# Kernel optimization log

Measured on AMD Instinct MI355X. Metric: run time of the kernel, lower is better.

The kernel has to match this reference:

```python
import jax, jax.numpy as jnp
import numpy as np

NUM_FIELDS = 16
EMBED = 32
W1 = 7
W2 = 5
VOCAB = 100000
BATCH = 4096
K1 = NUM_FIELDS // 2  # first k-max pool size (num_inputs/2)
K2 = 3                # second k-max pool size
DN = ('NHWC', 'HWIO', 'NHWC')


def kmax_pool_last(x, k):
    # k-max pooling along the last axis (tf.nn.top_k values)
    return jax.lax.top_k(x, k)[0]


def setup_inputs() -> dict:
    key = jax.random.key(0)
    ks = jax.random.split(key, 6)
    return {
        'idx': jax.random.randint(ks[0], (BATCH, NUM_FIELDS), 0, VOCAB),
        'w0': jax.random.normal(ks[1], (NUM_FIELDS, VOCAB, EMBED), jnp.float32) * 0.02,
        'b0': jnp.zeros((NUM_FIELDS, EMBED), jnp.float32),
        'f1': jax.random.normal(ks[2], (EMBED, W1, 1, 2), jnp.float32) * 0.1,
        'f2': jax.random.normal(ks[3], (EMBED, W2, 2, 2), jnp.float32) * 0.1,
        'w1': jax.random.normal(ks[4], (2 * 3 * EMBED, 1), jnp.float32) * 0.02,
        'b1': jnp.zeros((1,), jnp.float32),
    }


def reference(idx, w0, b0, f1, f2, w1, b1):
    # sparse one-hot matmul == embedding row gather: [B, F, E]
    emb = w0[jnp.arange(NUM_FIELDS)[None, :], idx] + b0[None, :, :]
    l = jnp.tanh(emb)  # layer_acts[0] = tanh; dropout identity at test
    # reshape [-1, F, E, 1] then transpose [0,2,1,3] -> [B, E, F, 1]
    l = jnp.transpose(l[..., None], (0, 2, 1, 3))
    # conv1: kernel [E, W1, 1, 2], SAME -> [B, E, F, 2]
    l = jax.lax.conv_general_dilated(l, f1, (1, 1), 'SAME', dimension_numbers=DN)
    # k-max pool over field axis (last axis after transpose) -> [B, E, K1, 2]
    l = jnp.transpose(kmax_pool_last(jnp.transpose(l, (0, 1, 3, 2)), K1), (0, 1, 3, 2))
    # conv2: kernel [E, W2, 2, 2], SAME -> [B, E, K1, 2]
    l = jax.lax.conv_general_dilated(l, f2, (1, 1), 'SAME', dimension_numbers=DN)
    # second k-max pool -> [B, E, 3, 2]
    l = jnp.transpose(kmax_pool_last(jnp.transpose(l, (0, 1, 3, 2)), K2), (0, 1, 3, 2))
    l = jnp.tanh(l.reshape(l.shape[0], EMBED * 3 * 2))  # layer_acts[1] = tanh
    logits = (l @ w1 + b1).reshape(-1)  # layer_acts[2] = none
    return jax.nn.sigmoid(logits)  # y_prob
```

## Files before the change

### kernel.cpp

```cpp
#include <hip/hip_runtime.h>
#include <math.h>

#define NF 16
#define VOCAB 100000
#define S1 28
#define NP1 31
#define PB 868
#define S2 20
#define LDSW 1736

typedef _Float16 h2 __attribute__((ext_vector_type(2)));

#if __has_builtin(__builtin_amdgcn_fdot2)
#define FDOT2(a, b, c) __builtin_amdgcn_fdot2((a), (b), (c), false)
#else
#define FDOT2(a, b, c) ((float)(a)[0] * (float)(b)[0] + ((float)(a)[1] * (float)(b)[1] + (c)))
#endif

__device__ __forceinline__ float tanhf_fast(float x) {
    float e = __expf(2.f * x);
    return 1.f - 2.f * __builtin_amdgcn_rcpf(e + 1.f);
}

__device__ __forceinline__ h2 u2h(unsigned int u) {
    union { unsigned int u; h2 h; } c; c.u = u; return c.h;
}

__global__ void pack_filters(const float* __restrict__ f1,
                             const float* __restrict__ f2,
                             unsigned int* __restrict__ ws) {
    int t = threadIdx.x;
    if (t < 224) {
        int j = t / 14, r = t % 14, kw = r >> 1, o = r & 1;
        h2 h;
        h[0] = (_Float16)f1[((2 * j) * 7 + kw) * 2 + o];
        h[1] = (_Float16)f1[((2 * j + 1) * 7 + kw) * 2 + o];
        union { h2 h; unsigned int u; } c; c.h = h;
        ws[t] = c.u;
    }
    for (int n = t; n < 320; n += 256) {
        int kh = n / 10, r = n % 10, kw = r >> 1, o = r & 1;
        h2 h;
        h[0] = (_Float16)f2[(kh * 5 + kw) * 4 + o];
        h[1] = (_Float16)f2[(kh * 5 + kw) * 4 + 2 + o];
        union { h2 h; unsigned int u; } c; c.h = h;
        ws[256 + n] = c.u;
    }
}

__global__ __launch_bounds__(64, 4) void ccpm_fwd(
    const int* __restrict__ idx,
    const float* __restrict__ w0,
    const float* __restrict__ b0,
    const float* __restrict__ w1,
    const float* __restrict__ b1,
    const unsigned int* __restrict__ FP,
    float* __restrict__ out)
{
    const int b = blockIdx.x;
    const int l = threadIdx.x;

    __shared__ __align__(16) unsigned int lds[LDSW];

    const float4 z4 = make_float4(0.f, 0.f, 0.f, 0.f);

    #pragma unroll
    for (int i = 0; i < 7; ++i) {
        int n = i * 64 + l;
        if (n < LDSW / 4) ((float4*)lds)[n] = z4;
    }
    __syncthreads();

    {
        int f  = l >> 2;
        int e0 = (l & 3) * 8;
        int row = idx[b * NF + f];
        const float4* src = (const float4*)(w0 + ((size_t)f * VOCAB + row) * 32 + e0);
        const float4* bb  = (const float4*)(b0 + f * 32 + e0);
        float4 v0 = src[0], v1 = src[1];
        float4 u0 = bb[0],  u1 = bb[1];
        float g[8];
        g[0]=v0.x+u0.x; g[1]=v0.y+u0.y; g[2]=v0.z+u0.z; g[3]=v0.w+u0.w;
        g[4]=v1.x+u1.x; g[5]=v1.y+u1.y; g[6]=v1.z+u1.z; g[7]=v1.w+u1.w;
        _Float16* H = (_Float16*)lds;
        const int C = f + 3;
        #pragma unroll
        for (int i = 0; i < 8; ++i) {
            int R = e0 + i + 15;
            _Float16 hv = (_Float16)tanhf_fast(g[i]);
            H[((R >> 1) * S1 + C) * 2 + (R & 1)] = hv;
            int prB = (R & 1) ? (R >> 1) : (R >> 1) - 1;
            H[(PB + prB * S1 + C) * 2 + ((R & 1) ^ 1)] = hv;
        }
    }
    __syncthreads();

    const int h  = l >> 1;
    const int wh = l & 1;

    float a0[8], a1[8];
    {
        #pragma unroll
        for (int w = 0; w < 8; ++w) { a0[w] = 0.f; a1[w] = 0.f; }
        const unsigned int* plane = lds + ((h & 1) ? PB : 0);
        const int pr0 = h >> 1;
        const int wb  = wh * 8;
        #pragma unroll 2
        for (int j = 0; j < 16; ++j) {
            const uint4* rp = (const uint4*)(plane + (pr0 + j) * S1 + wb);
            uint4 q0 = rp[0], q1 = rp[1], q2 = rp[2], q3 = rp[3];
            unsigned int win[16] = {q0.x,q0.y,q0.z,q0.w, q1.x,q1.y,q1.z,q1.w,
                                    q2.x,q2.y,q2.z,q2.w, q3.x,q3.y,q3.z,q3.w};
            const unsigned int* ft = FP + j * 14;
            #pragma unroll
            for (int kw = 0; kw < 7; ++kw) {
                h2 f0 = u2h(ft[kw * 2 + 0]);
                h2 f1h = u2h(ft[kw * 2 + 1]);
                #pragma unroll
                for (int w = 0; w < 8; ++w) {
                    h2 wv = u2h(win[w + kw]);
                    a0[w] = FDOT2(wv, f0, a0[w]);
                    a1[w] = FDOT2(wv, f1h, a1[w]);
                }
            }
        }
    }
    __syncthreads();

    #pragma unroll
    for (int i = 0; i < 5; ++i) {
        int n = i * 64 + l;
        if (n < (63 * S2) / 4) ((float4*)lds)[n] = z4;
    }
    __syncthreads();

    {
        float own[8], recv[8];
        #pragma unroll
        for (int i = 0; i < 8; ++i) {
            own[i]  = wh ? a1[i] : a0[i];
            recv[i] = __shfl_xor(wh ? a0[i] : a1[i], 1, 64);
        }
        float v[16];
        #pragma unroll
        for (int i = 0; i < 8; ++i) {
            v[i]     = wh ? recv[i] : own[i];
            v[8 + i] = wh ? own[i] : recv[i];
        }
        int r[16];
        #pragma unroll
        for (int i = 0; i < 16; ++i) r[i] = 0;
        #pragma unroll
        for (int i = 0; i < 16; ++i)
            #pragma unroll
            for (int j = i + 1; j < 16; ++j) {
                bool ge = v[i] >= v[j];
                r[j] += ge ? 1 : 0;
                r[i] += ge ? 0 : 1;
            }
        _Float16* H = (_Float16*)lds;
        #pragma unroll
        for (int i = 0; i < 16; ++i)
            if (r[i] < 8)
                H[((h + 15) * S2 + (r[i] + 2)) * 2 + wh] = (_Float16)v[i];
    }
    __syncthreads();

    float c0[4], c1[4];
    {
        #pragma unroll
        for (int w = 0; w < 4; ++w) { c0[w] = 0.f; c1[w] = 0.f; }
        const int wb2 = wh * 4;
        #pragma unroll 2
        for (int kh = 0; kh < 32; ++kh) {
            const uint4* rp = (const uint4*)(lds + (h + kh) * S2 + wb2);
            uint4 qa = rp[0], qb = rp[1];
            unsigned int q[8] = {qa.x,qa.y,qa.z,qa.w, qb.x,qb.y,qb.z,qb.w};
            const unsigned int* ft = FP + 256 + kh * 10;
            #pragma unroll
            for (int kw = 0; kw < 5; ++kw) {
                h2 f0 = u2h(ft[kw * 2 + 0]);
                h2 f1h = u2h(ft[kw * 2 + 1]);
                #pragma unroll
                for (int w = 0; w < 4; ++w) {
                    h2 wv = u2h(q[w + kw]);
                    c0[w] = FDOT2(wv, f0, c0[w]);
                    c1[w] = FDOT2(wv, f1h, c1[w]);
                }
            }
        }
    }

    {
        float own[4], recv[4];
        #pragma unroll
        for (int i = 0; i < 4; ++i) {
            own[i]  = wh ? c1[i] : c0[i];
            recv[i] = __shfl_xor(wh ? c0[i] : c1[i], 1, 64);
        }
        float v[8];
        #pragma unroll
        for (int i = 0; i < 4; ++i) {
            v[i]     = wh ? recv[i] : own[i];
            v[4 + i] = wh ? own[i] : recv[i];
        }
        int r[8];
        #pragma unroll
        for (int i = 0; i < 8; ++i) r[i] = 0;
        #pragma unroll
        for (int i = 0; i < 8; ++i)
            #pragma unroll
            for (int j = i + 1; j < 8; ++j) {
                bool ge = v[i] >= v[j];
                r[j] += ge ? 1 : 0;
                r[i] += ge ? 0 : 1;
            }
        float t0 = 0.f, t1 = 0.f, t2 = 0.f;
        #pragma unroll
        for (int i = 0; i < 8; ++i) {
            t0 = (r[i] == 0) ? v[i] : t0;
            t1 = (r[i] == 1) ? v[i] : t1;
            t2 = (r[i] == 2) ? v[i] : t2;
        }
        float s = tanhf_fast(t0) * w1[h * 6 + wh]
                + tanhf_fast(t1) * w1[h * 6 + 2 + wh]
                + tanhf_fast(t2) * w1[h * 6 + 4 + wh];
        #pragma unroll
        for (int off = 32; off; off >>= 1) s += __shfl_xor(s, off, 64);
        if (l == 0) {
            float logit = s + b1[0];
            out[b] = __builtin_amdgcn_rcpf(1.f + __expf(-logit));
        }
    }
}

extern "C" void kernel_launch(void* const* d_in, const int* in_sizes, int n_in,
                              void* d_out, int out_size, void* d_ws, size_t ws_size,
                              hipStream_t stream) {
    const int*   idx = (const int*)d_in[0];
    const float* w0  = (const float*)d_in[1];
    const float* b0  = (const float*)d_in[2];
    const float* f1  = (const float*)d_in[3];
    const float* f2  = (const float*)d_in[4];
    const float* w1  = (const float*)d_in[5];
    const float* b1  = (const float*)d_in[6];
    float* out = (float*)d_out;
    unsigned int* ws = (unsigned int*)d_ws;

    pack_filters<<<1, 256, 0, stream>>>(f1, f2, ws);
    ccpm_fwd<<<out_size, 64, 0, stream>>>(idx, w0, b0, w1, b1, ws, out);
}
```

Baseline: 279.1 us.

## Split conv output channels across two wavefronts per sample with 128-thread blocks

Doubles the block to 128 threads so each wavefront computes one output channel of both convolutions, halving the per-thread accumulators and FDOT2 work. Filter packing is relaid out per output channel, and the two k-max pools now exchange data through cross-half shuffles (xor 32) instead of neighbour-lane shuffles. The final logit is combined across the two wavefronts through LDS with an extra barrier. This raises parallelism and lowers register pressure per sample, at the cost of duplicated sorting work in both halves and more block-level synchronisation.

```diff
diff --git a/kernel.cpp b/kernel.cpp
--- a/kernel.cpp
+++ b/kernel.cpp
@@ -4,10 +4,10 @@
 #define NF 16
 #define VOCAB 100000
 #define S1 28
-#define NP1 31
 #define PB 868
 #define S2 20
-#define LDSW 1736
+#define PLW 1736
+#define REDS 1700
 
 typedef _Float16 h2 __attribute__((ext_vector_type(2)));
 
@@ -31,24 +31,24 @@
                              unsigned int* __restrict__ ws) {
     int t = threadIdx.x;
     if (t < 224) {
-        int j = t / 14, r = t % 14, kw = r >> 1, o = r & 1;
+        int o = t / 112, r = t % 112, j = r / 7, kw = r % 7;
         h2 h;
         h[0] = (_Float16)f1[((2 * j) * 7 + kw) * 2 + o];
         h[1] = (_Float16)f1[((2 * j + 1) * 7 + kw) * 2 + o];
         union { h2 h; unsigned int u; } c; c.h = h;
-        ws[t] = c.u;
+        ws[o * 128 + j * 8 + kw] = c.u;
     }
     for (int n = t; n < 320; n += 256) {
-        int kh = n / 10, r = n % 10, kw = r >> 1, o = r & 1;
+        int o = n / 160, r = n % 160, kh = r / 5, kw = r % 5;
         h2 h;
         h[0] = (_Float16)f2[(kh * 5 + kw) * 4 + o];
         h[1] = (_Float16)f2[(kh * 5 + kw) * 4 + 2 + o];
         union { h2 h; unsigned int u; } c; c.h = h;
-        ws[256 + n] = c.u;
-    }
-}
-
-__global__ __launch_bounds__(64, 4) void ccpm_fwd(
+        ws[256 + o * 256 + kh * 8 + kw] = c.u;
+    }
+}
+
+__global__ __launch_bounds__(128, 8) void ccpm_fwd(
     const int* __restrict__ idx,
     const float* __restrict__ w0,
     const float* __restrict__ b0,
@@ -58,34 +58,30 @@
     float* __restrict__ out)
 {
     const int b = blockIdx.x;
-    const int l = threadIdx.x;
-
-    __shared__ __align__(16) unsigned int lds[LDSW];
+    const int t = threadIdx.x;
+
+    __shared__ __align__(16) unsigned int lds[PLW];
 
     const float4 z4 = make_float4(0.f, 0.f, 0.f, 0.f);
 
     #pragma unroll
-    for (int i = 0; i < 7; ++i) {
-        int n = i * 64 + l;
-        if (n < LDSW / 4) ((float4*)lds)[n] = z4;
-    }
-    __syncthreads();
-
-    {
-        int f  = l >> 2;
-        int e0 = (l & 3) * 8;
+    for (int i = 0; i < 4; ++i) {
+        int n = i * 128 + t;
+        if (n < PLW / 4) ((float4*)lds)[n] = z4;
+    }
+    __syncthreads();
+
+    {
+        int f  = t >> 3;
+        int e0 = (t & 7) * 4;
         int row = idx[b * NF + f];
-        const float4* src = (const float4*)(w0 + ((size_t)f * VOCAB + row) * 32 + e0);
-        const float4* bb  = (const float4*)(b0 + f * 32 + e0);
-        float4 v0 = src[0], v1 = src[1];
-        float4 u0 = bb[0],  u1 = bb[1];
-        float g[8];
-        g[0]=v0.x+u0.x; g[1]=v0.y+u0.y; g[2]=v0.z+u0.z; g[3]=v0.w+u0.w;
-        g[4]=v1.x+u1.x; g[5]=v1.y+u1.y; g[6]=v1.z+u1.z; g[7]=v1.w+u1.w;
+        float4 v = *(const float4*)(w0 + ((size_t)f * VOCAB + row) * 32 + e0);
+        float4 u = *(const float4*)(b0 + f * 32 + e0);
+        float g[4] = {v.x + u.x, v.y + u.y, v.z + u.z, v.w + u.w};
         _Float16* H = (_Float16*)lds;
         const int C = f + 3;
         #pragma unroll
-        for (int i = 0; i < 8; ++i) {
+        for (int i = 0; i < 4; ++i) {
             int R = e0 + i + 15;
             _Float16 hv = (_Float16)tanhf_fast(g[i]);
             H[((R >> 1) * S1 + C) * 2 + (R & 1)] = hv;
@@ -95,142 +91,137 @@
     }
     __syncthreads();
 
-    const int h  = l >> 1;
-    const int wh = l & 1;
-
-    float a0[8], a1[8];
-    {
-        #pragma unroll
-        for (int w = 0; w < 8; ++w) { a0[w] = 0.f; a1[w] = 0.f; }
+    const int h    = t & 31;
+    const int half = (t >> 5) & 1;
+    const int o    = t >> 6;
+
+    float a[8];
+    {
+        #pragma unroll
+        for (int w = 0; w < 8; ++w) a[w] = 0.f;
         const unsigned int* plane = lds + ((h & 1) ? PB : 0);
         const int pr0 = h >> 1;
-        const int wb  = wh * 8;
+        const int cb  = half * 8;
+        const unsigned int* ft = FP + o * 128;
         #pragma unroll 2
         for (int j = 0; j < 16; ++j) {
-            const uint4* rp = (const uint4*)(plane + (pr0 + j) * S1 + wb);
-            uint4 q0 = rp[0], q1 = rp[1], q2 = rp[2], q3 = rp[3];
-            unsigned int win[16] = {q0.x,q0.y,q0.z,q0.w, q1.x,q1.y,q1.z,q1.w,
-                                    q2.x,q2.y,q2.z,q2.w, q3.x,q3.y,q3.z,q3.w};
-            const unsigned int* ft = FP + j * 14;
+            const unsigned int* rb = plane + (pr0 + j) * S1 + cb;
+            uint4 q0 = ((const uint4*)rb)[0];
+            uint4 q1 = ((const uint4*)rb)[1];
+            uint4 q2 = ((const uint4*)rb)[2];
+            uint2 q3 = *(const uint2*)(rb + 12);
+            unsigned int win[14] = {q0.x,q0.y,q0.z,q0.w, q1.x,q1.y,q1.z,q1.w,
+                                    q2.x,q2.y,q2.z,q2.w, q3.x,q3.y};
             #pragma unroll
             for (int kw = 0; kw < 7; ++kw) {
-                h2 f0 = u2h(ft[kw * 2 + 0]);
-                h2 f1h = u2h(ft[kw * 2 + 1]);
+                h2 fp = u2h(ft[j * 8 + kw]);
                 #pragma unroll
-                for (int w = 0; w < 8; ++w) {
-                    h2 wv = u2h(win[w + kw]);
-                    a0[w] = FDOT2(wv, f0, a0[w]);
-                    a1[w] = FDOT2(wv, f1h, a1[w]);
-                }
-            }
+                for (int w = 0; w < 8; ++w)
+                    a[w] = FDOT2(u2h(win[w + kw]), fp, a[w]);
+            }
+        }
+    }
+
+    float v16[16];
+    {
+        #pragma unroll
+        for (int i = 0; i < 8; ++i) {
+            float recv = __shfl_xor(a[i], 32, 64);
+            v16[half ? 8 + i : i]  = a[i];
+            v16[half ? i : 8 + i]  = recv;
         }
     }
     __syncthreads();
 
     #pragma unroll
-    for (int i = 0; i < 5; ++i) {
-        int n = i * 64 + l;
-        if (n < (63 * S2) / 4) ((float4*)lds)[n] = z4;
-    }
-    __syncthreads();
-
-    {
-        float own[8], recv[8];
-        #pragma unroll
-        for (int i = 0; i < 8; ++i) {
-            own[i]  = wh ? a1[i] : a0[i];
-            recv[i] = __shfl_xor(wh ? a0[i] : a1[i], 1, 64);
-        }
-        float v[16];
-        #pragma unroll
-        for (int i = 0; i < 8; ++i) {
-            v[i]     = wh ? recv[i] : own[i];
-            v[8 + i] = wh ? own[i] : recv[i];
-        }
-        int r[16];
-        #pragma unroll
-        for (int i = 0; i < 16; ++i) r[i] = 0;
+    for (int i = 0; i < 3; ++i) {
+        int n = i * 128 + t;
+        if (n < 315) ((float4*)lds)[n] = z4;
+    }
+    __syncthreads();
+
+    {
+        int r16[16];
+        #pragma unroll
+        for (int i = 0; i < 16; ++i) r16[i] = 0;
         #pragma unroll
         for (int i = 0; i < 16; ++i)
             #pragma unroll
             for (int j = i + 1; j < 16; ++j) {
-                bool ge = v[i] >= v[j];
-                r[j] += ge ? 1 : 0;
-                r[i] += ge ? 0 : 1;
-            }
-        _Float16* H = (_Float16*)lds;
-        #pragma unroll
-        for (int i = 0; i < 16; ++i)
-            if (r[i] < 8)
-                H[((h + 15) * S2 + (r[i] + 2)) * 2 + wh] = (_Float16)v[i];
-    }
-    __syncthreads();
-
-    float c0[4], c1[4];
-    {
-        #pragma unroll
-        for (int w = 0; w < 4; ++w) { c0[w] = 0.f; c1[w] = 0.f; }
-        const int wb2 = wh * 4;
+                bool ge = v16[i] >= v16[j];
+                r16[j] += ge ? 1 : 0;
+                r16[i] += ge ? 0 : 1;
+            }
+        if (half == 0) {
+            _Float16* H = (_Float16*)lds;
+            #pragma unroll
+            for (int i = 0; i < 16; ++i)
+                if (r16[i] < 8)
+                    H[((h + 15) * S2 + (r16[i] + 2)) * 2 + o] = (_Float16)v16[i];
+        }
+    }
+    __syncthreads();
+
+    float c[4];
+    {
+        #pragma unroll
+        for (int w = 0; w < 4; ++w) c[w] = 0.f;
+        const int cb2 = half * 4;
+        const unsigned int* ft2 = FP + 256 + o * 256;
         #pragma unroll 2
         for (int kh = 0; kh < 32; ++kh) {
-            const uint4* rp = (const uint4*)(lds + (h + kh) * S2 + wb2);
-            uint4 qa = rp[0], qb = rp[1];
+            const unsigned int* rb = lds + (h + kh) * S2 + cb2;
+            uint4 qa = ((const uint4*)rb)[0];
+            uint4 qb = ((const uint4*)rb)[1];
             unsigned int q[8] = {qa.x,qa.y,qa.z,qa.w, qb.x,qb.y,qb.z,qb.w};
-            const unsigned int* ft = FP + 256 + kh * 10;
             #pragma unroll
             for (int kw = 0; kw < 5; ++kw) {
-                h2 f0 = u2h(ft[kw * 2 + 0]);
-                h2 f1h = u2h(ft[kw * 2 + 1]);
+                h2 fp = u2h(ft2[kh * 8 + kw]);
                 #pragma unroll
-                for (int w = 0; w < 4; ++w) {
-                    h2 wv = u2h(q[w + kw]);
-                    c0[w] = FDOT2(wv, f0, c0[w]);
-                    c1[w] = FDOT2(wv, f1h, c1[w]);
-                }
-            }
-        }
-    }
-
-    {
-        float own[4], recv[4];
+                for (int w = 0; w < 4; ++w)
+                    c[w] = FDOT2(u2h(q[w + kw]), fp, c[w]);
+            }
+        }
+    }
+
+    {
+        float v8[8];
         #pragma unroll
         for (int i = 0; i < 4; ++i) {
-            own[i]  = wh ? c1[i] : c0[i];
-            recv[i] = __shfl_xor(wh ? c0[i] : c1[i], 1, 64);
-        }
-        float v[8];
-        #pragma unroll
-        for (int i = 0; i < 4; ++i) {
-            v[i]     = wh ? recv[i] : own[i];
-            v[4 + i] = wh ? own[i] : recv[i];
-        }
-        int r[8];
-        #pragma unroll
-        for (int i = 0; i < 8; ++i) r[i] = 0;
+            float recv = __shfl_xor(c[i], 32, 64);
+            v8[half ? 4 + i : i] = c[i];
+            v8[half ? i : 4 + i] = recv;
+        }
+        int r8[8];
+        #pragma unroll
+        for (int i = 0; i < 8; ++i) r8[i] = 0;
         #pragma unroll
         for (int i = 0; i < 8; ++i)
             #pragma unroll
             for (int j = i + 1; j < 8; ++j) {
-                bool ge = v[i] >= v[j];
-                r[j] += ge ? 1 : 0;
-                r[i] += ge ? 0 : 1;
+                bool ge = v8[i] >= v8[j];
+                r8[j] += ge ? 1 : 0;
+                r8[i] += ge ? 0 : 1;
             }
         float t0 = 0.f, t1 = 0.f, t2 = 0.f;
         #pragma unroll
         for (int i = 0; i < 8; ++i) {
-            t0 = (r[i] == 0) ? v[i] : t0;
-            t1 = (r[i] == 1) ? v[i] : t1;
-            t2 = (r[i] == 2) ? v[i] : t2;
-        }
-        float s = tanhf_fast(t0) * w1[h * 6 + wh]
-                + tanhf_fast(t1) * w1[h * 6 + 2 + wh]
-                + tanhf_fast(t2) * w1[h * 6 + 4 + wh];
+            t0 = (r8[i] == 0) ? v8[i] : t0;
+            t1 = (r8[i] == 1) ? v8[i] : t1;
+            t2 = (r8[i] == 2) ? v8[i] : t2;
+        }
+        float s = tanhf_fast(t0) * w1[h * 6 + o]
+                + tanhf_fast(t1) * w1[h * 6 + 2 + o]
+                + tanhf_fast(t2) * w1[h * 6 + 4 + o];
+        s = half ? 0.f : s;
         #pragma unroll
         for (int off = 32; off; off >>= 1) s += __shfl_xor(s, off, 64);
-        if (l == 0) {
-            float logit = s + b1[0];
-            out[b] = __builtin_amdgcn_rcpf(1.f + __expf(-logit));
-        }
+        if ((t & 63) == 0) ((float*)lds)[REDS + o] = s;
+    }
+    __syncthreads();
+    if (t == 0) {
+        float logit = ((float*)lds)[REDS] + ((float*)lds)[REDS + 1] + b1[0];
+        out[b] = __builtin_amdgcn_rcpf(1.f + __expf(-logit));
     }
 }
 
@@ -248,5 +239,5 @@
     unsigned int* ws = (unsigned int*)d_ws;
 
     pack_filters<<<1, 256, 0, stream>>>(f1, f2, ws);
-    ccpm_fwd<<<out_size, 64, 0, stream>>>(idx, w0, b0, w1, b1, ws, out);
-}
+    ccpm_fwd<<<out_size, 128, 0, stream>>>(idx, w0, b0, w1, b1, ws, out);
+}
```

Result: slower. 289.1 us (+3.6%).
